# Kernel tuning notes

Measured on AMD Instinct MI355X. Metric: run time of the kernel, lower is better.

The kernel has to match this reference:

```python
import jax, jax.numpy as jnp
import numpy as np


def _shift_kernel(dtype=jnp.float32):
    # IdealDelayKernels: 9 output channels, 8 one-hot 3x3 shift taps (center skipped), 9th all-zero
    k = np.zeros((9, 1, 1, 3, 3), np.float32)
    idx = -1
    for i in range(3):
        for j in range(3):
            if i == 1 and j == 1:
                continue
            idx += 1
            k[idx, 0, 0, i, j] = 1.0
    return jnp.asarray(k, dtype)


def _conv2d(x, w, b, pad):
    y = jax.lax.conv_general_dilated(x, w, (1, 1), [(pad, pad), (pad, pad)],
                                     dimension_numbers=('NCHW', 'OIHW', 'NCHW'))
    return y if b is None else y + b[None, :, None, None]


def setup_inputs() -> dict:
    key = jax.random.key(0)
    ks = jax.random.split(key, 16)
    B, C, H, W = 2, 19, 512, 512
    s = 0.1  # xavier-ish scale for small convs
    return {
        'x': jax.random.normal(ks[0], (B, C, H, W), jnp.float32),
        'image': jax.random.normal(ks[1], (B, 3, H, W), jnp.float32),
        # IntraNetwork(3 -> 16 -> 16 -> 19): conv3x3, conv3x3, conv1x1 (BN frozen at identity)
        'intra_w1': jax.random.normal(ks[2], (16, 3, 3, 3), jnp.float32) * s,
        'intra_b1': jnp.zeros((16,), jnp.float32),
        'intra_w2': jax.random.normal(ks[3], (16, 16, 3, 3), jnp.float32) * s,
        'intra_b2': jnp.zeros((16,), jnp.float32),
        'intra_w3': jax.random.normal(ks[4], (19, 16, 1, 1), jnp.float32) * s,
        'intra_b3': jnp.zeros((19,), jnp.float32),
        # GuidingNetwork(20 -> 32 -> 32 -> 11): conv3x3, conv3x3, conv1x1 + sigmoid
        'guide_w1': jax.random.normal(ks[5], (32, 20, 3, 3), jnp.float32) * s,
        'guide_b1': jnp.zeros((32,), jnp.float32),
        'guide_w2': jax.random.normal(ks[6], (32, 32, 3, 3), jnp.float32) * s,
        'guide_b2': jnp.zeros((32,), jnp.float32),
        'guide_w3': jax.random.normal(ks[7], (11, 32, 1, 1), jnp.float32) * s,
        'guide_b3': jnp.zeros((11,), jnp.float32),
    }


def reference(x, image, intra_w1, intra_b1, intra_w2, intra_b2, intra_w3, intra_b3,
              guide_w1, guide_b1, guide_w2, guide_b2, guide_w3, guide_b3):
    # intra_net: image -> [B,19,H,W] (frozen BN == identity)
    f = jax.nn.relu(_conv2d(image, intra_w1, intra_b1, 1))
    f = jax.nn.relu(_conv2d(f, intra_w2, intra_b2, 1))
    intra = _conv2d(f, intra_w3, intra_b3, 0)            # [B,19,H,W]

    # Laplacian edge on the argmax label map
    single_x = jnp.argmax(x, axis=1, keepdims=True).astype(x.dtype)  # [B,1,H,W]
    lapla = jnp.full((1, 1, 3, 3), 1.0, x.dtype).at[0, 0, 1, 1].set(-8.0)
    edge = _conv2d(single_x, lapla, None, 1)             # [B,1,H,W]

    # guiding network: cat(intra, edge) -> 11 per-pixel guide weights
    gi = jnp.concatenate([intra, edge], axis=1)          # [B,20,H,W]
    g = jax.nn.relu(_conv2d(gi, guide_w1, guide_b1, 1))
    g = jax.nn.relu(_conv2d(g, guide_w2, guide_b2, 1))
    g = jax.nn.sigmoid(_conv2d(g, guide_w3, guide_b3, 0))  # [B,11,H,W]
    guide_feat = g[:, :, None]                           # [B,11,1,H,W]
    guide_feat = guide_feat / (jnp.sum(guide_feat, axis=1, keepdims=True) + 1e-9)

    # shift-kernel conv3d: [B,1,19,H,W] -> [B,9,19,H,W]
    xs = x[:, None]
    short = jax.lax.conv_general_dilated(xs, _shift_kernel(x.dtype), (1, 1, 1),
                                         [(0, 0), (1, 1), (1, 1)],
                                         dimension_numbers=('NCDHW', 'OIDHW', 'NCDHW'))
    xcat = jnp.concatenate([xs, short, intra[:, None]], axis=1)  # [B,11,19,H,W]

    out = jnp.sum(guide_feat * xcat, axis=1)             # [B,19,H,W]
    return (out, guide_feat, edge)
```

## Files before the change

### kernel.cpp

```cpp
#include <hip/hip_runtime.h>
#include <math.h>

constexpr int H = 512, W = 512, B = 2;
constexpr int HW = H * W;

typedef __attribute__((ext_vector_type(8))) short short8;
typedef __attribute__((ext_vector_type(4))) float floatx4;
typedef __attribute__((ext_vector_type(4))) unsigned int uint4v;

__device__ inline unsigned short f2bf(float f) {
  union { float f; unsigned int u; } x{f};
  const unsigned int u = x.u;
  return (unsigned short)((u + 0x7FFFu + ((u >> 16) & 1u)) >> 16);
}
__device__ inline float bf2f(unsigned short s) {
  union { unsigned int u; float f; } x;
  x.u = (unsigned int)s << 16;
  return x.f;
}
__device__ inline void unpk2(unsigned int u, float& lo, float& hi) {
  union { unsigned int u; float f; } a, b;
  a.u = u << 16;
  b.u = u & 0xffff0000u;
  lo = a.f;
  hi = b.f;
}

__device__ inline void load_row3(const float* __restrict__ plane, int hh,
                                 int w, float r[3]) {
  r[0] = 0.f; r[1] = 0.f; r[2] = 0.f;
  if ((unsigned)hh < (unsigned)H) {
    const float* rp = plane + (size_t)hh * W + w;
    r[1] = rp[0];
    if (w > 0) r[0] = rp[-1];
    if (w + 1 < W) r[2] = rp[1];
  }
}

template <int CIN, int COUT, bool RELU>
__global__ __launch_bounds__(256) void conv3x3_fp32_pack(
    const float* __restrict__ in0, const float* __restrict__ wgt,
    const float* __restrict__ bias, unsigned short* __restrict__ outp) {
  constexpr int TS = 16, TH = 18, LDW = 20;
  __shared__ float tile[CIN][TH][LDW];
  const int tx = threadIdx.x, ty = threadIdx.y;
  const int tid = ty * 16 + tx;
  const int w0 = blockIdx.x * TS, h0 = blockIdx.y * TS, b = blockIdx.z;

  for (int idx = tid; idx < CIN * TH * TH; idx += 256) {
    const int cin = idx / (TH * TH);
    const int rem = idx - cin * (TH * TH);
    const int r = rem / TH, c = rem - r * TH;
    const int gh = h0 + r - 1, gw = w0 + c - 1;
    float v = 0.f;
    if ((unsigned)gh < (unsigned)H && (unsigned)gw < (unsigned)W)
      v = in0[(size_t)(b * CIN + cin) * HW + gh * W + gw];
    tile[cin][r][c] = v;
  }
  __syncthreads();

  float acc[COUT];
#pragma unroll
  for (int co = 0; co < COUT; ++co) acc[co] = bias[co];
  for (int cin = 0; cin < CIN; ++cin) {
#pragma unroll
    for (int t = 0; t < 9; ++t) {
      const int ky = t / 3, kx = t - ky * 3;
      const float v = tile[cin][ty + ky][tx + kx];
#pragma unroll
      for (int co = 0; co < COUT; ++co)
        acc[co] = fmaf(v, wgt[(co * CIN + cin) * 9 + t], acc[co]);
    }
  }
  const int oh = h0 + ty, ow = w0 + tx;
  unsigned int pk[COUT / 2];
#pragma unroll
  for (int c2 = 0; c2 < COUT / 2; ++c2) {
    float a0 = acc[2 * c2], a1 = acc[2 * c2 + 1];
    if (RELU) { a0 = fmaxf(a0, 0.f); a1 = fmaxf(a1, 0.f); }
    pk[c2] = (unsigned)f2bf(a0) | ((unsigned)f2bf(a1) << 16);
  }
  unsigned short* dst = outp + ((size_t)(b * H + oh) * W + ow) * COUT;
#pragma unroll
  for (int u = 0; u < COUT / 8; ++u)
    *(uint4v*)(dst + u * 8) = uint4v{pk[u * 4], pk[u * 4 + 1], pk[u * 4 + 2], pk[u * 4 + 3]};
}

template <int CIN, int CINP, int COUT, int KS>
__device__ inline void repack_body(int idx, const float* __restrict__ w,
                                   unsigned short* __restrict__ bp) {
  constexpr int NT = COUT / 16;
  if (idx >= NT * KS * 512) return;
  const int j = idx & 7;
  const int l = (idx >> 3) & 63;
  const int ks = (idx >> 9) % KS;
  const int nt = idx / (KS * 512);
  const int co = nt * 16 + (l & 15);
  const int kglob = ks * 32 + (l >> 4) * 8 + j;
  const int tap = kglob / CINP;
  const int cin = kglob % CINP;
  float v = 0.f;
  if (tap < 9 && cin < CIN) v = w[((size_t)co * CIN + cin) * 9 + tap];
  bp[idx] = f2bf(v);
}

__global__ __launch_bounds__(256) void repack_all(
    const float* __restrict__ iw2, const float* __restrict__ gw1,
    const float* __restrict__ gw2, unsigned short* __restrict__ bp_ic2,
    unsigned short* __restrict__ bp_gc1, unsigned short* __restrict__ bp_gc2) {
  const int blk = blockIdx.x, tid = threadIdx.x;
  if (blk < 10) {
    repack_body<16, 16, 16, 5>(blk * 256 + tid, iw2, bp_ic2);
  } else if (blk < 38) {
    repack_body<20, 24, 32, 7>((blk - 10) * 256 + tid, gw1, bp_gc1);
  } else {
    repack_body<32, 32, 32, 9>((blk - 38) * 256 + tid, gw2, bp_gc2);
  }
}

template <int CINP, int KS, int NT, bool EDGE19, int EPI>
__global__ __launch_bounds__(256) void conv3x3_mfma(
    const unsigned short* __restrict__ inp, const float* __restrict__ edg,
    const unsigned short* __restrict__ bpack, const float* __restrict__ bias,
    const float* __restrict__ ew, const float* __restrict__ eb,
    unsigned short* __restrict__ outp, float* __restrict__ outf,
    const float* __restrict__ xin, const unsigned short* __restrict__ ipn,
    float* __restrict__ outc) {
  constexpr int COUT = NT * 16;
  constexpr int CS = (CINP == 16) ? 24 : 40;
  constexpr int EPS = (EPI == 1) ? 24 : 40;
  constexpr int TR = 10;
  constexpr int XN = 19 * 10 * 34;
  constexpr int XIT = (XN + 255) / 256;
  __shared__ __align__(16) unsigned short tile[TR * 34 * CS];

  const int tid = threadIdx.x;
  const int w0 = blockIdx.x * 32, h0 = blockIdx.y * 8, b = blockIdx.z;

  for (int idx = tid; idx < TR * 34; idx += 256) {
    const int r = idx / 34, c = idx - r * 34;
    const int gh = h0 + r - 1, gw = w0 + c - 1;
    unsigned short* dst = tile + (size_t)(r * 34 + c) * CS;
    if ((unsigned)gh < (unsigned)H && (unsigned)gw < (unsigned)W) {
      const unsigned short* src = inp + ((size_t)(b * H + gh) * W + gw) * CINP;
#pragma unroll
      for (int u = 0; u < CINP / 8; ++u)
        *(uint4v*)(dst + u * 8) = *(const uint4v*)(src + u * 8);
      if (EDGE19) {
        const float* sp = edg + (size_t)b * HW;
        float r0[3], r1[3], r2[3];
        load_row3(sp, gh - 1, gw, r0);
        load_row3(sp, gh, gw, r1);
        load_row3(sp, gh + 1, gw, r2);
        const float e = r0[0] + r0[1] + r0[2] + r1[0] + r1[2] + r2[0] +
                        r2[1] + r2[2] - 8.f * r1[1];
        dst[19] = f2bf(e);
        outf[(size_t)b * HW + (size_t)gh * W + gw] = e;
      }
    } else {
#pragma unroll
      for (int u = 0; u < CINP / 8; ++u)
        *(uint4v*)(dst + u * 8) = uint4v{0, 0, 0, 0};
    }
  }
  __syncthreads();

  float xr[EPI == 3 ? XIT : 1];
  if constexpr (EPI == 3) {
#pragma unroll
    for (int i = 0; i < XIT; ++i) {
      const int idx = tid + i * 256;
      float v = 0.f;
      if (idx < XN) {
        const int c = idx / 340;
        const int rem = idx - c * 340;
        const int r = rem / 34, col = rem - r * 34;
        const int gh2 = h0 + r - 1, gw2 = w0 + col - 1;
        if ((unsigned)gh2 < (unsigned)H && (unsigned)gw2 < (unsigned)W)
          v = xin[(size_t)(b * 19 + c) * HW + (size_t)gh2 * W + gw2];
      }
      xr[i] = v;
    }
  }

  const int wv = tid >> 6, lane = tid & 63;
  const int q = lane >> 4, l15 = lane & 15;
  const int rb = wv * 2;

  floatx4 acc[4][NT];
#pragma unroll
  for (int mf = 0; mf < 4; ++mf)
#pragma unroll
    for (int nt = 0; nt < NT; ++nt) acc[mf][nt] = floatx4{0.f, 0.f, 0.f, 0.f};

#pragma unroll
  for (int ks = 0; ks < KS; ++ks) {
    short8 bfrag[NT];
#pragma unroll
    for (int nt = 0; nt < NT; ++nt)
      bfrag[nt] = *(const short8*)(bpack + (size_t)(((nt * KS) + ks) * 64 + lane) * 8);

    const int kbase = ks * 32;
    const int kq = kbase + q * 8;
    int tapq = kq / CINP;
    const int cinq = kq % CINP;
    if (tapq > 8) tapq = 8;
    const int ky = tapq / 3, kx = tapq - ky * 3;
    const unsigned short* aptr =
        tile + (size_t)((rb + ky) * 34 + (l15 + kx)) * CS + cinq;

#pragma unroll
    for (int mf = 0; mf < 4; ++mf) {
      constexpr int mfs[4][2] = {{0, 0}, {0, 16}, {1, 0}, {1, 16}};
      const int off = (mfs[mf][0] * 34 + mfs[mf][1]) * CS;
      const short8 af = *(const short8*)(aptr + off);
#pragma unroll
      for (int nt = 0; nt < NT; ++nt)
        acc[mf][nt] = __builtin_amdgcn_mfma_f32_16x16x32_bf16(
            af, bfrag[nt], acc[mf][nt], 0, 0, 0);
    }
  }

  if constexpr (EPI == 0) {
#pragma unroll
    for (int nt = 0; nt < NT; ++nt) {
      const float bv = bias[nt * 16 + l15];
#pragma unroll
      for (int mf = 0; mf < 4; ++mf) {
        const int row = mf >> 1, colb = (mf & 1) * 16 + q * 4;
        unsigned short* dst =
            outp + ((size_t)(b * H + h0 + rb + row) * W + w0) * COUT + nt * 16 + l15;
#pragma unroll
        for (int rg = 0; rg < 4; ++rg) {
          const float v = fmaxf(acc[mf][nt][rg] + bv, 0.f);
          dst[(size_t)(colb + rg) * COUT] = f2bf(v);
        }
      }
    }
  } else {
    __syncthreads();
#pragma unroll
    for (int nt = 0; nt < NT; ++nt) {
      const float bv = bias[nt * 16 + l15];
#pragma unroll
      for (int mf = 0; mf < 4; ++mf) {
        const int row = rb + (mf >> 1), colb = (mf & 1) * 16 + q * 4;
#pragma unroll
        for (int rg = 0; rg < 4; ++rg) {
          const int px = row * 32 + colb + rg;
          tile[(size_t)px * EPS + nt * 16 + l15] =
              f2bf(fmaxf(acc[mf][nt][rg] + bv, 0.f));
        }
      }
    }
    __syncthreads();

    {
      const int p = tid;
      const int gh = h0 + (p >> 5), gw = w0 + (p & 31);
      const unsigned short* src = tile + (size_t)p * EPS;

      if constexpr (EPI == 1) {
        float xi[16];
        const uint4v r0 = *(const uint4v*)src;
        const uint4v r1 = *(const uint4v*)(src + 8);
        unpk2(r0.x, xi[0], xi[1]);   unpk2(r0.y, xi[2], xi[3]);
        unpk2(r0.z, xi[4], xi[5]);   unpk2(r0.w, xi[6], xi[7]);
        unpk2(r1.x, xi[8], xi[9]);   unpk2(r1.y, xi[10], xi[11]);
        unpk2(r1.z, xi[12], xi[13]); unpk2(r1.w, xi[14], xi[15]);
        float a[19];
#pragma unroll
        for (int co = 0; co < 19; ++co) a[co] = eb[co];
#pragma unroll
        for (int c = 0; c < 16; ++c) {
          const float v = xi[c];
#pragma unroll
          for (int co = 0; co < 19; ++co) a[co] = fmaf(v, ew[co * 16 + c], a[co]);
        }
        unsigned int pk[12];
#pragma unroll
        for (int j = 0; j < 9; ++j)
          pk[j] = (unsigned)f2bf(a[2 * j]) | ((unsigned)f2bf(a[2 * j + 1]) << 16);
        pk[9] = (unsigned)f2bf(a[18]);
        pk[10] = 0; pk[11] = 0;
        unsigned short* dst = outp + ((size_t)(b * H + gh) * W + gw) * 24;
#pragma unroll
        for (int u = 0; u < 3; ++u)
          *(uint4v*)(dst + u * 8) =
              uint4v{pk[u * 4], pk[u * 4 + 1], pk[u * 4 + 2], pk[u * 4 + 3]};
      } else {
        float xi[32];
#pragma unroll
        for (int u = 0; u < 4; ++u) {
          const uint4v r = *(const uint4v*)(src + u * 8);
          unpk2(r.x, xi[u * 8 + 0], xi[u * 8 + 1]);
          unpk2(r.y, xi[u * 8 + 2], xi[u * 8 + 3]);
          unpk2(r.z, xi[u * 8 + 4], xi[u * 8 + 5]);
          unpk2(r.w, xi[u * 8 + 6], xi[u * 8 + 7]);
        }

        if constexpr (EPI == 3) {
          __syncthreads();
          float* xs = (float*)tile;
#pragma unroll
          for (int i = 0; i < XIT; ++i) {
            const int idx = tid + i * 256;
            if (idx < XN) xs[idx] = xr[i];
          }
        }

        float g[11], sum = 0.f;
#pragma unroll
        for (int co = 0; co < 11; ++co) {
          float a = eb[co];
#pragma unroll
          for (int c = 0; c < 32; ++c) a = fmaf(xi[c], ew[co * 32 + c], a);
          g[co] = 1.f / (1.f + expf(-a));
          sum += g[co];
        }
        const float inv = 1.f / (sum + 1e-9f);
        const size_t s = (size_t)gh * W + gw;
#pragma unroll
        for (int co = 0; co < 11; ++co)
          outf[(size_t)(b * 11 + co) * HW + s] = g[co] * inv;

        if constexpr (EPI == 3) {
          __syncthreads();

          float gn[11];
#pragma unroll
          for (int m = 0; m < 11; ++m) gn[m] = g[m] * inv;
          float* xs = (float*)tile;
          const int pr = p >> 5, pc = p & 31;
          const unsigned short* ip = ipn + ((size_t)b * HW + s) * 24;
          for (int c = 0; c < 19; ++c) {
            const float* xc = xs + c * 340;
            const float* x0 = xc + (pr + 0) * 34 + pc;
            const float* x1 = xc + (pr + 1) * 34 + pc;
            const float* x2 = xc + (pr + 2) * 34 + pc;
            const float itv = bf2f(ip[c]);
            float a = gn[0] * x1[1];
            a = fmaf(gn[1], x0[0], a);
            a = fmaf(gn[2], x0[1], a);
            a = fmaf(gn[3], x0[2], a);
            a = fmaf(gn[4], x1[0], a);
            a = fmaf(gn[5], x1[2], a);
            a = fmaf(gn[6], x2[0], a);
            a = fmaf(gn[7], x2[1], a);
            a = fmaf(gn[8], x2[2], a);
            a = fmaf(gn[10], itv, a);
            outc[(size_t)(b * 19 + c) * HW + s] = a;
          }
        }
      }
    }
  }
}

__global__ __launch_bounds__(256) void argmax_kernel(
    const float* __restrict__ x, float* __restrict__ sx) {
  const int t = blockIdx.x * 256 + threadIdx.x;
  const int b = t >> 18;
  const int s = t & (HW - 1);
  const float* xp = x + (size_t)b * 19 * HW + s;
  float bv = *xp;
  float ix = 0.f;
#pragma unroll
  for (int c = 1; c < 19; ++c) {
    const float v = xp[(size_t)c * HW];
    if (v > bv) { bv = v; ix = (float)c; }
  }
  sx[(size_t)b * HW + s] = ix;
}

extern "C" void kernel_launch(void* const* d_in, const int* in_sizes, int n_in,
                              void* d_out, int out_size, void* d_ws,
                              size_t ws_size, hipStream_t stream) {
  const float* x     = (const float*)d_in[0];
  const float* image = (const float*)d_in[1];
  const float* iw1 = (const float*)d_in[2];
  const float* ib1 = (const float*)d_in[3];
  const float* iw2 = (const float*)d_in[4];
  const float* ib2 = (const float*)d_in[5];
  const float* iw3 = (const float*)d_in[6];
  const float* ib3 = (const float*)d_in[7];
  const float* gw1 = (const float*)d_in[8];
  const float* gb1 = (const float*)d_in[9];
  const float* gw2 = (const float*)d_in[10];
  const float* gb2 = (const float*)d_in[11];
  const float* gw3 = (const float*)d_in[12];
  const float* gb3 = (const float*)d_in[13];

  float* ws = (float*)d_ws;
  float* sx = ws;
  unsigned short* f1p  = (unsigned short*)(ws + (size_t)2 * HW);
  unsigned short* intp = (unsigned short*)(ws + (size_t)34 * HW);
  unsigned short* g1p  = (unsigned short*)(ws + (size_t)58 * HW);
  unsigned short* bp_ic2 = (unsigned short*)(ws + (size_t)122 * HW);
  unsigned short* bp_gc1 = bp_ic2 + 4096;
  unsigned short* bp_gc2 = bp_gc1 + 12288;

  float* out0 = (float*)d_out;
  float* gfo  = out0 + (size_t)2 * 19 * HW;
  float* edg  = gfo + (size_t)2 * 11 * HW;

  const dim3 blk16(16, 16);
  const dim3 grd16(W / 16, H / 16, B);
  const dim3 grdM(W / 32, H / 8, B);
  const int flat1 = (B * HW) / 256;

  argmax_kernel<<<flat1, 256, 0, stream>>>(x, sx);
  repack_all<<<74, 256, 0, stream>>>(iw2, gw1, gw2, bp_ic2, bp_gc1, bp_gc2);

  conv3x3_fp32_pack<3, 16, true><<<grd16, blk16, 0, stream>>>(image, iw1, ib1, f1p);
  conv3x3_mfma<16, 5, 1, false, 1><<<grdM, 256, 0, stream>>>(
      f1p, nullptr, bp_ic2, ib2, iw3, ib3, intp, nullptr, nullptr, nullptr, nullptr);
  conv3x3_mfma<24, 7, 2, true, 0><<<grdM, 256, 0, stream>>>(
      intp, sx, bp_gc1, gb1, nullptr, nullptr, g1p, edg, nullptr, nullptr, nullptr);
  conv3x3_mfma<32, 9, 2, false, 3><<<grdM, 256, 0, stream>>>(
      g1p, nullptr, bp_gc2, gb2, gw3, gb3, nullptr, gfo, x, intp, out0);
}
```

Measured before the change: 224.8 us.

## Restructure final epilogue: channel-interleaved x tile, deferred x loads, vector intra reads

```diff
diff --git a/kernel.cpp b/kernel.cpp
--- a/kernel.cpp
+++ b/kernel.cpp
@@ -132,7 +132,9 @@
   constexpr int TR = 10;
   constexpr int XN = 19 * 10 * 34;
   constexpr int XIT = (XN + 255) / 256;
-  __shared__ __align__(16) unsigned short tile[TR * 34 * CS];
+  constexpr int CPC = 22;
+  constexpr int CSX = (EPI == 3) ? 44 : CS;
+  __shared__ __align__(16) unsigned short tile[TR * 34 * CSX];
 
   const int tid = threadIdx.x;
   const int w0 = blockIdx.x * 32, h0 = blockIdx.y * 8, b = blockIdx.z;
@@ -165,24 +167,6 @@
   }
   __syncthreads();
 
-  float xr[EPI == 3 ? XIT : 1];
-  if constexpr (EPI == 3) {
-#pragma unroll
-    for (int i = 0; i < XIT; ++i) {
-      const int idx = tid + i * 256;
-      float v = 0.f;
-      if (idx < XN) {
-        const int c = idx / 340;
-        const int rem = idx - c * 340;
-        const int r = rem / 34, col = rem - r * 34;
-        const int gh2 = h0 + r - 1, gw2 = w0 + col - 1;
-        if ((unsigned)gh2 < (unsigned)H && (unsigned)gw2 < (unsigned)W)
-          v = xin[(size_t)(b * 19 + c) * HW + (size_t)gh2 * W + gw2];
-      }
-      xr[i] = v;
-    }
-  }
-
   const int wv = tid >> 6, lane = tid & 63;
   const int q = lane >> 4, l15 = lane & 15;
   const int rb = wv * 2;
@@ -260,7 +244,12 @@
       const int gh = h0 + (p >> 5), gw = w0 + (p & 31);
       const unsigned short* src = tile + (size_t)p * EPS;
 
-      if constexpr (EPI == 1) {
+      if constexpr (EPI == 4) {
+        unsigned short* dst = outp + ((size_t)(b * H + gh) * W + gw) * 32;
+#pragma unroll
+        for (int u = 0; u < 4; ++u)
+          *(uint4v*)(dst + u * 8) = *(const uint4v*)(src + u * 8);
+      } else if constexpr (EPI == 1) {
         float xi[16];
         const uint4v r0 = *(const uint4v*)src;
         const uint4v r1 = *(const uint4v*)(src + 8);
@@ -298,16 +287,24 @@
           unpk2(r.z, xi[u * 8 + 4], xi[u * 8 + 5]);
           unpk2(r.w, xi[u * 8 + 6], xi[u * 8 + 7]);
         }
-
-        if constexpr (EPI == 3) {
-          __syncthreads();
-          float* xs = (float*)tile;
-#pragma unroll
-          for (int i = 0; i < XIT; ++i) {
-            const int idx = tid + i * 256;
-            if (idx < XN) xs[idx] = xr[i];
+        __syncthreads();
+
+        float xr[XIT];
+#pragma unroll
+        for (int i = 0; i < XIT; ++i) {
+          const int idx = tid + i * 256;
+          float v = 0.f;
+          if (idx < XN) {
+            const int c = idx / 340;
+            const int rem = idx - c * 340;
+            const int r = rem / 34, col = rem - r * 34;
+            const int gh2 = h0 + r - 1, gw2 = w0 + col - 1;
+            if ((unsigned)gh2 < (unsigned)H && (unsigned)gw2 < (unsigned)W)
+              v = xin[(size_t)(b * 19 + c) * HW + (size_t)gh2 * W + gw2];
           }
-        }
+          xr[i] = v;
+        }
+        asm volatile("" ::: "memory");
 
         float g[11], sum = 0.f;
 #pragma unroll
@@ -324,33 +321,57 @@
         for (int co = 0; co < 11; ++co)
           outf[(size_t)(b * 11 + co) * HW + s] = g[co] * inv;
 
-        if constexpr (EPI == 3) {
-          __syncthreads();
-
-          float gn[11];
-#pragma unroll
-          for (int m = 0; m < 11; ++m) gn[m] = g[m] * inv;
-          float* xs = (float*)tile;
-          const int pr = p >> 5, pc = p & 31;
-          const unsigned short* ip = ipn + ((size_t)b * HW + s) * 24;
-          for (int c = 0; c < 19; ++c) {
-            const float* xc = xs + c * 340;
-            const float* x0 = xc + (pr + 0) * 34 + pc;
-            const float* x1 = xc + (pr + 1) * 34 + pc;
-            const float* x2 = xc + (pr + 2) * 34 + pc;
-            const float itv = bf2f(ip[c]);
-            float a = gn[0] * x1[1];
-            a = fmaf(gn[1], x0[0], a);
-            a = fmaf(gn[2], x0[1], a);
-            a = fmaf(gn[3], x0[2], a);
-            a = fmaf(gn[4], x1[0], a);
-            a = fmaf(gn[5], x1[2], a);
-            a = fmaf(gn[6], x2[0], a);
-            a = fmaf(gn[7], x2[1], a);
-            a = fmaf(gn[8], x2[2], a);
-            a = fmaf(gn[10], itv, a);
-            outc[(size_t)(b * 19 + c) * HW + s] = a;
+        float* xs = (float*)tile;
+#pragma unroll
+        for (int i = 0; i < XIT; ++i) {
+          const int idx = tid + i * 256;
+          if (idx < XN) {
+            const int c = idx / 340;
+            const int rem = idx - c * 340;
+            const int r = rem / 34, col = rem - r * 34;
+            xs[(r * 34 + col) * CPC + c] = xr[i];
           }
+        }
+        __syncthreads();
+
+        float gn[11];
+#pragma unroll
+        for (int m = 0; m < 11; ++m) gn[m] = g[m] * inv;
+        const int pr = p >> 5, pc = p & 31;
+
+        constexpr int taps[9][3] = {{1, 1, 0}, {0, 0, 1}, {0, 1, 2},
+                                    {0, 2, 3}, {1, 0, 4}, {1, 2, 5},
+                                    {2, 0, 6}, {2, 1, 7}, {2, 2, 8}};
+        float a[19];
+#pragma unroll
+        for (int t = 0; t < 9; ++t) {
+          const float gv = gn[taps[t][2]];
+          const float* xp =
+              xs + ((pr + taps[t][0]) * 34 + (pc + taps[t][1])) * CPC;
+#pragma unroll
+          for (int j = 0; j < 9; ++j) {
+            const float2 v = *(const float2*)(xp + 2 * j);
+            if (t == 0) {
+              a[2 * j] = gv * v.x;
+              a[2 * j + 1] = gv * v.y;
+            } else {
+              a[2 * j] = fmaf(gv, v.x, a[2 * j]);
+              a[2 * j + 1] = fmaf(gv, v.y, a[2 * j + 1]);
+            }
+          }
+          if (t == 0) a[18] = gv * xp[18];
+          else a[18] = fmaf(gv, xp[18], a[18]);
+        }
+        const unsigned short* ip = ipn + ((size_t)b * HW + s) * 24;
+        const uint4v i0 = *(const uint4v*)ip;
+        const uint4v i1 = *(const uint4v*)(ip + 8);
+        const uint4v i2 = *(const uint4v*)(ip + 16);
+        unsigned short itv[24];
+        *(uint4v*)itv = i0; *(uint4v*)(itv + 8) = i1; *(uint4v*)(itv + 16) = i2;
+#pragma unroll
+        for (int c = 0; c < 19; ++c) {
+          a[c] = fmaf(gn[10], bf2f(itv[c]), a[c]);
+          outc[(size_t)(b * 19 + c) * HW + s] = a[c];
         }
       }
     }
@@ -415,7 +436,7 @@
   conv3x3_fp32_pack<3, 16, true><<<grd16, blk16, 0, stream>>>(image, iw1, ib1, f1p);
   conv3x3_mfma<16, 5, 1, false, 1><<<grdM, 256, 0, stream>>>(
       f1p, nullptr, bp_ic2, ib2, iw3, ib3, intp, nullptr, nullptr, nullptr, nullptr);
-  conv3x3_mfma<24, 7, 2, true, 0><<<grdM, 256, 0, stream>>>(
+  conv3x3_mfma<24, 7, 2, true, 4><<<grdM, 256, 0, stream>>>(
       intp, sx, bp_gc1, gb1, nullptr, nullptr, g1p, edg, nullptr, nullptr, nullptr);
   conv3x3_mfma<32, 9, 2, false, 3><<<grdM, 256, 0, stream>>>(
       g1p, nullptr, bp_gc2, gb2, gw3, gb3, nullptr, gfo, x, intp, out0);
```

Measured after the change: 237.9 us. 5.8% more time.
